# Optimization experiments

Measured on AMD Instinct MI355X. Metric: run time of the kernel, lower is better.

Reference implementation:

```python
import jax, jax.numpy as jnp
import numpy as np

DEPTH = 6; HEADS = 6; DIM = 384; HD = DIM // HEADS
WS = 14; WINDOW_BLOCKS = (0, 1, 3, 4)
IMG = 512; PATCH = 16; GRID = IMG // PATCH        # 32x32 token grid
PRE_GRID = 14                                      # 224 // 16 pretrain grid
SCALE = HD ** -0.5


def layer_norm(x, w, b, eps=1e-5):
    u = x.mean(-1, keepdims=True)
    s = ((x - u) ** 2).mean(-1, keepdims=True)
    return (x - u) / jnp.sqrt(s + eps) * w + b


def get_rel_pos(size, rel_pos):
    # q_size == k_size here; relative coords in [0, 2*size-2]
    coords = jnp.arange(size)[:, None] - jnp.arange(size)[None, :] + (size - 1)
    return rel_pos[coords]  # (size, size, HD)


def attention(x, qkv_w, qkv_b, proj_w, proj_b, rel_h, rel_w):
    B, H, W, C = x.shape
    N = H * W
    qkv = (x.reshape(B, N, C) @ qkv_w.T + qkv_b).reshape(B, N, 3, HEADS, HD)
    qkv = jnp.moveaxis(qkv, 2, 0).transpose(0, 1, 3, 2, 4)  # (3,B,h,N,d)
    q, k, v = qkv[0], qkv[1], qkv[2]
    attn = jnp.einsum('bhqd,bhkd->bhqk', q * SCALE, k)
    # decomposed relative position bias (ViTDet add_decomposed_rel_pos)
    Rh = get_rel_pos(H, rel_h)  # (H,H,d)
    Rw = get_rel_pos(W, rel_w)  # (W,W,d)
    rq = q.reshape(B, HEADS, H, W, HD)
    bias_h = jnp.einsum('bnhwc,hkc->bnhwk', rq, Rh)  # (B,h,H,W,H)
    bias_w = jnp.einsum('bnhwc,wkc->bnhwk', rq, Rw)  # (B,h,H,W,W)
    attn = (attn.reshape(B, HEADS, H, W, H, W)
            + bias_h[..., :, None] + bias_w[..., None, :]).reshape(B, HEADS, N, N)
    attn = jax.nn.softmax(attn, axis=-1)
    out = jnp.einsum('bhqk,bhkd->bhqd', attn, v)
    out = out.transpose(0, 2, 1, 3).reshape(B, H, W, C)
    return out @ proj_w.T + proj_b


def window_partition(x, ws):
    B, H, W, C = x.shape
    pad_h = (ws - H % ws) % ws
    pad_w = (ws - W % ws) % ws
    x = jnp.pad(x, ((0, 0), (0, pad_h), (0, pad_w), (0, 0)))
    Hp, Wp = H + pad_h, W + pad_w
    x = x.reshape(B, Hp // ws, ws, Wp // ws, ws, C)
    x = x.transpose(0, 1, 3, 2, 4, 5).reshape(-1, ws, ws, C)
    return x, Hp, Wp


def window_unpartition(win, ws, Hp, Wp, H, W):
    B = win.shape[0] // ((Hp // ws) * (Wp // ws))
    x = win.reshape(B, Hp // ws, Wp // ws, ws, ws, -1)
    x = x.transpose(0, 1, 3, 2, 4, 5).reshape(B, Hp, Wp, -1)
    return x[:, :H, :W]


def block(x, p, windowed):
    shortcut = x
    x = layer_norm(x, p['n1w'], p['n1b'])
    if windowed:
        H, W = x.shape[1], x.shape[2]
        x, Hp, Wp = window_partition(x, WS)
    x = attention(x, p['qw'], p['qb'], p['pw'], p['pb'], p['rh'], p['rw'])
    if windowed:
        x = window_unpartition(x, WS, Hp, Wp, H, W)
    x = shortcut + x
    h = layer_norm(x, p['n2w'], p['n2b'])
    h = jax.nn.gelu(h @ p['f1w'].T + p['f1b'], approximate=False)
    return x + h @ p['f2w'].T + p['f2b']


def vit_forward(x, patch_w, patch_b, pos_embed, norm1_w, norm1_b, qkv_w, qkv_b,
                proj_w, proj_b, norm2_w, norm2_b, fc1_w, fc1_b, fc2_w, fc2_b,
                rel_pos_h, rel_pos_w):
    y = jax.lax.conv_general_dilated(
        x, patch_w, (PATCH, PATCH), 'VALID',
        dimension_numbers=('NCHW', 'OIHW', 'NCHW'))
    y = y.transpose(0, 2, 3, 1) + patch_b  # (B, GRID, GRID, DIM)
    # abs pos embed: bicubic resize from pretrain 14x14 grid to 32x32
    pos = pos_embed.reshape(1, PRE_GRID, PRE_GRID, DIM)
    pos = jax.image.resize(pos, (1, GRID, GRID, DIM), 'bicubic')
    y = y + pos
    for i in range(DEPTH):
        windowed = i in WINDOW_BLOCKS
        L = 2 * WS - 1 if windowed else 2 * GRID - 1
        p = dict(n1w=norm1_w[i], n1b=norm1_b[i], qw=qkv_w[i], qb=qkv_b[i],
                 pw=proj_w[i], pb=proj_b[i], rh=rel_pos_h[i, :L], rw=rel_pos_w[i, :L],
                 n2w=norm2_w[i], n2b=norm2_b[i], f1w=fc1_w[i], f1b=fc1_b[i],
                 f2w=fc2_w[i], f2b=fc2_b[i])
        y = block(y, p, windowed)
    return y.transpose(0, 3, 1, 2)  # (B, DIM, GRID, GRID) 'last_feat'


def setup_inputs() -> dict:
    key = jax.random.key(0)
    ks = jax.random.split(key, 10)
    B = 4
    std = 0.02
    f32 = jnp.float32
    return {
        'x': jax.random.normal(ks[0], (B, 3, IMG, IMG), f32),
        'patch_w': jax.random.normal(ks[1], (DIM, 3, PATCH, PATCH), f32) * 0.05,
        'patch_b': jnp.zeros((DIM,), f32),
        'pos_embed': jax.random.normal(ks[2], (1, PRE_GRID * PRE_GRID, DIM), f32) * std,
        'norm1_w': jnp.ones((DEPTH, DIM), f32),
        'norm1_b': jnp.zeros((DEPTH, DIM), f32),
        'qkv_w': jax.random.normal(ks[3], (DEPTH, 3 * DIM, DIM), f32) * std,
        'qkv_b': jnp.zeros((DEPTH, 3 * DIM), f32),
        'proj_w': jax.random.normal(ks[4], (DEPTH, DIM, DIM), f32) * std,
        'proj_b': jnp.zeros((DEPTH, DIM), f32),
        'norm2_w': jnp.ones((DEPTH, DIM), f32),
        'norm2_b': jnp.zeros((DEPTH, DIM), f32),
        'fc1_w': jax.random.normal(ks[5], (DEPTH, 4 * DIM, DIM), f32) * std,
        'fc1_b': jnp.zeros((DEPTH, 4 * DIM), f32),
        'fc2_w': jax.random.normal(ks[6], (DEPTH, DIM, 4 * DIM), f32) * std,
        'fc2_b': jnp.zeros((DEPTH, DIM), f32),
        'rel_pos_h': jax.random.normal(ks[7], (DEPTH, 2 * GRID - 1, HD), f32) * std,
        'rel_pos_w': jax.random.normal(ks[8], (DEPTH, 2 * GRID - 1, HD), f32) * std,
    }


def reference(x, patch_w, patch_b, pos_embed, norm1_w, norm1_b, qkv_w, qkv_b,
              proj_w, proj_b, norm2_w, norm2_b, fc1_w, fc1_b, fc2_w, fc2_b,
              rel_pos_h, rel_pos_w):
    return vit_forward(x, patch_w, patch_b, pos_embed, norm1_w, norm1_b, qkv_w, qkv_b,
                       proj_w, proj_b, norm2_w, norm2_b, fc1_w, fc1_b, fc2_w, fc2_b,
                       rel_pos_h, rel_pos_w)
```

## Files before the change

### kernel.cpp

```cpp
#include <hip/hip_runtime.h>
#include <hip/hip_bf16.h>
#include <math.h>

#define B_SZ 4
#define DIM 384
#define HEADS 6
#define HD 64
#define NTOK 4096
#define WS 14
#define NWIN 36
#define WTOK 196

typedef unsigned short u16;
typedef __bf16 bf16_t;
typedef bf16_t bf16x8 __attribute__((ext_vector_type(8)));
typedef float f32x4 __attribute__((ext_vector_type(4)));

__device__ __forceinline__ float bf2f(unsigned u) { return __uint_as_float(u << 16); }
__device__ __forceinline__ u16 f2bf(float f) {
    unsigned u = __float_as_uint(f);
    unsigned r = (u + 0x7fffu + ((u >> 16) & 1u)) >> 16;
    return (u16)r;
}
__device__ __forceinline__ unsigned pk2bf(float a, float b) {
    __hip_bfloat162 h = __float22bfloat162_rn(make_float2(a, b));
    unsigned r; __builtin_memcpy(&r, &h, 4); return r;
}

__device__ __forceinline__ void ldsload16(const u16* g, u16* l) {
    __builtin_amdgcn_global_load_lds(
        (const __attribute__((address_space(1))) unsigned int*)g,
        (__attribute__((address_space(3))) unsigned int*)l, 16, 0, 0);
}

__device__ __forceinline__ int swz(int r) { return (r ^ (r >> 2)) & 3; }

__device__ inline float cubic_keys(float x) {
    x = fabsf(x);
    if (x <= 1.f) return ((1.5f * x - 2.5f) * x) * x + 1.f;
    if (x < 2.f)  return ((-0.5f * x + 2.5f) * x - 4.f) * x + 2.f;
    return 0.f;
}

__global__ __launch_bounds__(256) void setup_kernel(
        const float* __restrict__ p0, const float* __restrict__ p1,
        const float* __restrict__ p2, const float* __restrict__ p3,
        const float* __restrict__ p4, const float* __restrict__ p5,
        u16* __restrict__ wb, const float* __restrict__ pe,
        float* __restrict__ posr, const float* __restrict__ x,
        u16* __restrict__ col) {
    int i = (blockIdx.x * 256 + threadIdx.x) * 4;
    if (i < 10918656) {
        const float* s; int off;
        if      (i <   294912) { s = p0; off = 0; }
        else if (i <  2949120) { s = p1; off = 294912; }
        else if (i <  3833856) { s = p2; off = 2949120; }
        else if (i <  7372800) { s = p3; off = 3833856; }
        else if (i < 10911744) { s = p4; off = 7372800; }
        else                   { s = p5; off = 10911744; }
        float4 v = *(const float4*)(s + (i - off));
        u16 o[4] = { f2bf(v.x), f2bf(v.y), f2bf(v.z), f2bf(v.w) };
        *(uint2*)(wb + i) = *(const uint2*)o;
        return;
    }
    i -= 10918656;
    if (i < 393216) {
        int c = i % 384;
        int g = i / 384;
        int gy = g / 32, gx = g % 32;
        float wy[14], wx[14];
        float sy = (gy + 0.5f) * (14.f / 32.f) - 0.5f;
        float sx = (gx + 0.5f) * (14.f / 32.f) - 0.5f;
        float toty = 0.f, totx = 0.f;
        #pragma unroll
        for (int k = 0; k < 14; ++k) {
            wy[k] = cubic_keys(sy - (float)k); toty += wy[k];
            wx[k] = cubic_keys(sx - (float)k); totx += wx[k];
        }
        float4 acc = {0.f, 0.f, 0.f, 0.f};
        #pragma unroll 1
        for (int iy = 0; iy < 14; ++iy) {
            if (wy[iy] == 0.f) continue;
            float4 row = {0.f, 0.f, 0.f, 0.f};
            for (int ix = 0; ix < 14; ++ix) {
                if (wx[ix] == 0.f) continue;
                float4 pv = *(const float4*)(pe + (iy * 14 + ix) * 384 + c);
                row.x += wx[ix] * pv.x; row.y += wx[ix] * pv.y;
                row.z += wx[ix] * pv.z; row.w += wx[ix] * pv.w;
            }
            acc.x += wy[iy] * row.x; acc.y += wy[iy] * row.y;
            acc.z += wy[iy] * row.z; acc.w += wy[iy] * row.w;
        }
        float inv = 1.f / (toty * totx);
        acc.x *= inv; acc.y *= inv; acc.z *= inv; acc.w *= inv;
        *(float4*)(posr + i) = acc;
        return;
    }
    i -= 393216;
    if (i < 3145728) {
        int kk = i % 768;
        int p  = i / 768;
        int b  = p / 1024;
        int ph = (p % 1024) / 32;
        int pw = p % 32;
        int c = kk / 256;
        int r = kk % 256;
        int ii = r / 16, j = r % 16;
        float4 v = *(const float4*)(x + (size_t)b * 3 * 512 * 512 +
                                    (size_t)c * 512 * 512 +
                                    (size_t)(ph * 16 + ii) * 512 + (pw * 16 + j));
        u16 o[4] = { f2bf(v.x), f2bf(v.y), f2bf(v.z), f2bf(v.w) };
        *(uint2*)(col + i) = *(const uint2*)o;
    }
}

__global__ __launch_bounds__(256) void epi_ln_kernel(const float* __restrict__ P,
        const float* __restrict__ bias, const float* __restrict__ posr,
        float* __restrict__ y, int addy, int nsk,
        const float* __restrict__ lw, const float* __restrict__ lb,
        u16* __restrict__ lnout)
{
    int tok = blockIdx.x * 4 + (threadIdx.x >> 6);
    int t = threadIdx.x & 63;
    size_t base = (size_t)tok * 384;
    float v[6];
    float s = 0.f;
    #pragma unroll
    for (int i = 0; i < 6; ++i) {
        int c = t + 64 * i;
        float val = bias[c];
        #pragma unroll 1
        for (int sk = 0; sk < nsk; ++sk)
            val += P[(size_t)sk * 1572864 + base + c];
        if (posr) val += posr[(size_t)(tok & 1023) * 384 + c];
        if (addy) val += y[base + c];
        v[i] = val; s += val;
    }
    #pragma unroll
    for (int i = 0; i < 6; ++i) y[base + t + 64 * i] = v[i];
    if (!lnout) return;
    #pragma unroll
    for (int off = 32; off > 0; off >>= 1) s += __shfl_xor(s, off);
    float mean = s * (1.f / 384.f);
    float vs = 0.f;
    #pragma unroll
    for (int i = 0; i < 6; ++i) { float d = v[i] - mean; vs += d * d; }
    #pragma unroll
    for (int off = 32; off > 0; off >>= 1) vs += __shfl_xor(vs, off);
    float inv = rsqrtf(vs * (1.f / 384.f) + 1e-5f);
    u16* orow = lnout + base;
    #pragma unroll
    for (int i = 0; i < 6; ++i) {
        int c = t + 64 * i;
        orow[c] = f2bf((v[i] - mean) * inv * lw[c] + lb[c]);
    }
}

__global__ __launch_bounds__(256) void out_transpose(const float* __restrict__ y,
        float* __restrict__ outT)
{
    __shared__ float T[64][65];
    int c0 = blockIdx.x * 64, m0 = blockIdx.y * 64;
    int t = threadIdx.x;
    int cl = t & 63, wv = t >> 6;
    #pragma unroll
    for (int r = 0; r < 16; ++r) {
        int ml = wv * 16 + r;
        T[ml][cl] = y[(size_t)(m0 + ml) * 384 + c0 + cl];
    }
    __syncthreads();
    int b = m0 >> 10, g0 = m0 & 1023;
    int gl = t & 63;
    #pragma unroll
    for (int r = 0; r < 16; ++r) {
        int ccl = wv * 16 + r;
        outT[((size_t)(b * 384 + c0 + ccl)) * 1024 + g0 + gl] = T[gl][ccl];
    }
}

__global__ __launch_bounds__(256) void mfma_gemm4(
        const u16* __restrict__ A, const u16* __restrict__ Wt,
        const float* __restrict__ bias,
        float* __restrict__ outf, u16* __restrict__ outb,
        float* __restrict__ outp,
        int M, int N, int K, int act, int ksplit)
{
    __shared__ u16 As[2][8192];
    __shared__ u16 Bs[2][4096];
    int t = threadIdx.x;
    int lane = t & 63, wave = t >> 6;
    int wm = (wave >> 1) * 64, wn = (wave & 1) * 32;
    int m0 = blockIdx.y * 128, n0 = blockIdx.x * 64;
    int ks = blockIdx.z * ksplit;

    int r0 = t >> 2,        c0 = ((t & 3) ^ swz(t >> 2)) * 8;
    int r1 = 64 + (t >> 2), c1 = ((t & 3) ^ swz(64 + (t >> 2))) * 8;
    const u16* a0 = A + (size_t)(m0 + r0) * K + c0;
    const u16* a1 = A + (size_t)(m0 + r1) * K + c1;
    const u16* b0 = Wt + (size_t)(n0 + r0) * K + c0;

    auto stage = [&](int k0, int buf) {
        ldsload16(a0 + k0,      &As[buf][wave * 512]);
        ldsload16(a1 + k0,      &As[buf][2048 + wave * 512]);
        ldsload16(b0 + k0,      &Bs[buf][wave * 512]);
        ldsload16(a0 + k0 + 32, &As[buf][4096 + wave * 512]);
        ldsload16(a1 + k0 + 32, &As[buf][6144 + wave * 512]);
        ldsload16(b0 + k0 + 32, &Bs[buf][2048 + wave * 512]);
    };

    f32x4 acc[4][2] = {};
    int row_a = wm + (lane & 15);
    int row_b = wn + (lane & 15);
    int lq = lane >> 4;
    int nchunks = ksplit / 64;

    stage(ks, 0);
    __syncthreads();

    for (int ci = 0; ci < nchunks; ++ci) {
        int p = ci & 1;
        bool pref = (ci + 1 < nchunks);
        if (pref) stage(ks + (ci + 1) * 64, 1 - p);
        #pragma unroll
        for (int hf = 0; hf < 2; ++hf) {
            bf16x8 af[4], bfr[2];
            #pragma unroll
            for (int i = 0; i < 4; ++i) {
                int r = row_a + i * 16;
                af[i] = *(const bf16x8*)&As[p][hf * 4096 + r * 32 + ((lq ^ swz(r)) * 8)];
            }
            #pragma unroll
            for (int j = 0; j < 2; ++j) {
                int r = row_b + j * 16;
                bfr[j] = *(const bf16x8*)&Bs[p][hf * 2048 + r * 32 + ((lq ^ swz(r)) * 8)];
            }
            #pragma unroll
            for (int i = 0; i < 4; ++i)
                #pragma unroll
                for (int j = 0; j < 2; ++j)
                    acc[i][j] = __builtin_amdgcn_mfma_f32_16x16x32_bf16(
                        af[i], bfr[j], acc[i][j], 0, 0, 0);
        }
        if (pref) __syncthreads();
    }

    int colq = lane & 15, rowq = (lane >> 4) * 4;
    if (outp) {
        float* pp = outp + (size_t)blockIdx.z * M * N;
        #pragma unroll
        for (int i = 0; i < 4; ++i) {
            #pragma unroll
            for (int rr = 0; rr < 4; ++rr) {
                int m = m0 + wm + i * 16 + rowq + rr;
                size_t mo = (size_t)m * N;
                #pragma unroll
                for (int j = 0; j < 2; ++j) {
                    int n = n0 + wn + j * 16 + colq;
                    pp[mo + n] = acc[i][j][rr];
                }
            }
        }
        return;
    }
    #pragma unroll
    for (int i = 0; i < 4; ++i) {
        #pragma unroll
        for (int rr = 0; rr < 4; ++rr) {
            int m = m0 + wm + i * 16 + rowq + rr;
            size_t mo = (size_t)m * N;
            #pragma unroll
            for (int j = 0; j < 2; ++j) {
                int n = n0 + wn + j * 16 + colq;
                float v = acc[i][j][rr] + bias[n];
                if (act)  v = 0.5f * v * (1.f + erff(v * 0.70710678118654752f));
                if (outf) outf[mo + n] = v;
                if (outb) outb[mo + n] = f2bf(v);
            }
        }
    }
}

template<int N, int W>
__global__ __launch_bounds__(256) void attn_mfma(const u16* __restrict__ qkv,
        const u16* __restrict__ qkb, const float* __restrict__ rh,
        const float* __restrict__ rw, u16* __restrict__ outb,
        float* __restrict__ opart, float* __restrict__ lpart)
{
    constexpr int JS = (W == 32) ? 64 : 32;
    constexpr int L  = (W == 32) ? 63 : 27;
    constexpr int CTR = W - 1;
    constexpr int KSPAN = (W == 32) ? 512 : 224;
    constexpr int NKT = KSPAN / 32;
    __shared__ u16 KV[11776];
    __shared__ u16 bhl[64 * 66];
    __shared__ u16 bwl[64 * 66];
    __shared__ u16 Qt[64 * 66];

    u16* Pb = KV + 9216;
    u16* Rt = KV;

    int t = threadIdx.x, lane = t & 63, wave = t >> 6;
    int quad = lane >> 4, l15 = lane & 15;
    int uh = blockIdx.x, qb0 = blockIdx.y * 64;
    int z = (W == 32) ? blockIdx.z : 0;
    int kstart = z * KSPAN;
    int h = uh % HEADS, u = uh / HEADS;
    size_t tbase = (size_t)u * 1024;
    int wb_ = u / 9, wr = u - wb_ * 9;
    int wy = wr / 3, wx = wr - wy * 3;

    auto tok14 = [&](int iy, int ix) -> const u16* {
        int gy = wy * WS + iy, gx = wx * WS + ix;
        if (gy < 32 && gx < 32)
            return qkv + (size_t)(wb_ * 1024 + gy * 32 + gx) * 1152;
        return qkb;
    };
    auto rowptr = [&](int lq2) -> const u16* {
        if constexpr (W == 32) {
            return qkv + (tbase + lq2) * 1152;
        } else {
            int iy = lq2 / WS, ix = lq2 - iy * WS;
            return tok14(iy, ix);
        }
    };

    {
        int q = t & 63, ch0 = (t >> 6) * 16;
        int qc = qb0 + q; if (qc >= N) qc = N - 1;
        const u16* qp = rowptr(qc) + h * 64 + ch0;
        uint4 a = *(const uint4*)qp;
        uint4 b = *(const uint4*)(qp + 8);
        u16 vals[16];
        *(uint4*)vals = a; *(uint4*)(vals + 8) = b;
        #pragma unroll
        for (int c = 0; c < 16; ++c)
            Qt[(ch0 + c) * 66 + q] = ((qb0 + q) < N) ? vals[c] : (u16)0;
    }

    #pragma unroll
    for (int table = 0; table < 2; ++table) {
        __syncthreads();
        const float* tab = table ? rw : rh;
        for (int idx = t; idx < JS * 8; idx += 256) {
            int j = idx >> 3, cc0 = (idx & 7) * 8;
            u16 tmp[8];
            if (j < L) {
                const float* src = tab + (size_t)j * 64 + cc0;
                #pragma unroll
                for (int c = 0; c < 8; ++c) tmp[c] = f2bf(src[c]);
            } else {
                #pragma unroll
                for (int c = 0; c < 8; ++c) tmp[c] = 0;
            }
            *(uint4*)&Rt[j * 72 + cc0] = *(uint4*)tmp;
        }
        __syncthreads();
        if (wave < JS / 16) {
            int jt = wave;
            bf16x8 af0 = *(const bf16x8*)&Rt[(jt * 16 + l15) * 72 + quad * 8];
            bf16x8 af1 = *(const bf16x8*)&Rt[(jt * 16 + l15) * 72 + 32 + quad * 8];
            u16* dst = table ? bwl : bhl;
            #pragma unroll
            for (int qt = 0; qt < 4; ++qt) {
                bf16x8 qf0, qf1;
                u16* p0 = (u16*)&qf0; u16* p1 = (u16*)&qf1;
                #pragma unroll
                for (int zz = 0; zz < 8; ++zz) {
                    p0[zz] = Qt[(quad * 8 + zz) * 66 + qt * 16 + l15];
                    p1[zz] = Qt[(32 + quad * 8 + zz) * 66 + qt * 16 + l15];
                }
                f32x4 acc = {};
                acc = __builtin_amdgcn_mfma_f32_16x16x32_bf16(af0, qf0, acc, 0, 0, 0);
                acc = __builtin_amdgcn_mfma_f32_16x16x32_bf16(af1, qf1, acc, 0, 0, 0);
                #pragma unroll
                for (int r = 0; r < 4; ++r)
                    dst[(qt * 16 + l15) * 66 + jt * 16 + quad * 4 + r] = f2bf(acc[r]);
            }
        }
    }
    __syncthreads();

    int skey = (wave * 64 + lane) >> 3;
    int sc8  = ((wave * 64 + lane) & 7) ^ (skey & 7);
    int vkey = t & 31, vch0 = (t >> 5) * 8;
    int siy = 0, six = 0, viy = 0, vix = 0;
    if constexpr (W != 32) {
        int k0 = kstart + skey;
        siy = k0 / WS; six = k0 - siy * WS;
        int k1 = kstart + vkey;
        viy = k1 / WS; vix = k1 - viy * WS;
    }
    auto adv = [](int& iy, int& ix) { ix += 4; iy += 2; if (ix >= WS) { ix -= WS; ++iy; } };

    {
        const u16* kp = (W == 32) ? qkv + (tbase + kstart + skey) * 1152
                                  : tok14(siy, six);
        ldsload16(kp + 384 + h * 64 + sc8 * 8, KV + wave * 512);
        const u16* vp = (W == 32) ? qkv + (tbase + kstart + vkey) * 1152
                                  : tok14(viy, vix);
        uint4 vv = *(const uint4*)(vp + 768 + h * 64 + vch0);
        u16 tmp[8]; *(uint4*)tmp = vv;
        u16* vdst = KV + 4096;
        #pragma unroll
        for (int c = 0; c < 8; ++c) vdst[(vch0 + c) * 40 + vkey] = tmp[c];
        if constexpr (W != 32) { adv(siy, six); adv(viy, vix); }
    }

    bf16x8 qf[2];
    #pragma unroll
    for (int hc = 0; hc < 2; ++hc) {
        u16* qv = (u16*)&qf[hc];
        #pragma unroll
        for (int j = 0; j < 8; ++j)
            qv[j] = Qt[(hc * 32 + quad * 8 + j) * 66 + wave * 16 + l15];
    }
    int qme = wave * 16 + l15;
    bool wactive = (W == 32) ? true : ((qb0 + wave * 16) < N);
    int qq = qb0 + qme; if (qq >= N) qq = N - 1;
    int qh = qq / W, qw = qq - qh * W;
    float bwreg[2][4];
    int kh_[2][4], kw_[2][4];
    #pragma unroll
    for (int kc2 = 0; kc2 < 2; ++kc2)
        #pragma unroll
        for (int r = 0; r < 4; ++r) {
            int keyl = kc2 * 16 + quad * 4 + r;
            if constexpr (W == 32) {
                bwreg[kc2][r] = bf2f(bwl[qme * 66 + (qw - keyl + CTR)]);
            } else {
                kh_[kc2][r] = keyl / WS;
                kw_[kc2][r] = keyl - kh_[kc2][r] * WS;
            }
        }

    f32x4 of[4] = {};
    float lsum = 0.f;
    __syncthreads();

    for (int kt = 0; kt < NKT; ++kt) {
        int kb = kstart + kt * 32;
        int p = kt & 1;
        const u16* ksp = KV + p * 2048;
        const u16* vtp = KV + 4096 + p * 2560;
        bool pref = (kt + 1 < NKT);
        uint4 vpref;
        if (pref) {
            const u16* kp = (W == 32) ? qkv + (tbase + kb + 32 + skey) * 1152
                                      : tok14(siy, six);
            ldsload16(kp + 384 + h * 64 + sc8 * 8, KV + (1 - p) * 2048 + wave * 512);
            const u16* vp = (W == 32) ? qkv + (tbase + kb + 32 + vkey) * 1152
                                      : tok14(viy, vix);
            vpref = *(const uint4*)(vp + 768 + h * 64 + vch0);
            if constexpr (W != 32) { adv(siy, six); adv(viy, vix); }
        }

        if (wactive) {
            f32x4 st[2] = {};
            #pragma unroll
            for (int hc = 0; hc < 2; ++hc) {
                #pragma unroll
                for (int kc2 = 0; kc2 < 2; ++kc2) {
                    int key = kc2 * 16 + l15;
                    int c8 = hc * 4 + quad;
                    int pp = key * 8 + (c8 ^ (key & 7));
                    bf16x8 kf = *(const bf16x8*)&ksp[pp * 8];
                    st[kc2] = __builtin_amdgcn_mfma_f32_16x16x32_bf16(
                        kf, qf[hc], st[kc2], 0, 0, 0);
                }
            }
            float bh_t = 0.f;
            if constexpr (W == 32) bh_t = bf2f(bhl[qme * 66 + (qh - (kb >> 5) + CTR)]);
            #pragma unroll
            for (int kc2 = 0; kc2 < 2; ++kc2) {
                float pv4[4];
                #pragma unroll
                for (int r = 0; r < 4; ++r) {
                    int keyl = kc2 * 16 + quad * 4 + r;
                    float b;
                    if constexpr (W == 32) {
                        b = bh_t + bwreg[kc2][r];
                    } else {
                        b = bf2f(bhl[qme * 66 + (qh - kh_[kc2][r] + CTR)]) +
                            bf2f(bwl[qme * 66 + (qw - kw_[kc2][r] + CTR)]);
                    }
                    float pv = __expf(fmaf(st[kc2][r], 0.125f, b));
                    if (kb + keyl >= N) pv = 0.f;
                    lsum += pv;
                    pv4[r] = pv;
                }
                uint2 pk;
                pk.x = pk2bf(pv4[0], pv4[1]);
                pk.y = pk2bf(pv4[2], pv4[3]);
                *(uint2*)&Pb[wave * 640 + l15 * 40 + kc2 * 16 + quad * 4] = pk;
            }
            if constexpr (W != 32) {
                #pragma unroll
                for (int kc2 = 0; kc2 < 2; ++kc2)
                    #pragma unroll
                    for (int r = 0; r < 4; ++r) {
                        kw_[kc2][r] += 4; kh_[kc2][r] += 2;
                        if (kw_[kc2][r] >= WS) { kw_[kc2][r] -= WS; ++kh_[kc2][r]; }
                    }
            }
            bf16x8 pf = *(const bf16x8*)&Pb[wave * 640 + l15 * 40 + quad * 8];
            #pragma unroll
            for (int ca = 0; ca < 4; ++ca) {
                bf16x8 vf = *(const bf16x8*)&vtp[(ca * 16 + l15) * 40 + quad * 8];
                of[ca] = __builtin_amdgcn_mfma_f32_16x16x32_bf16(
                    vf, pf, of[ca], 0, 0, 0);
            }
        }

        if (pref) {
            u16 tmp[8]; *(uint4*)tmp = vpref;
            u16* vdst = KV + 4096 + (1 - p) * 2560;
            #pragma unroll
            for (int c = 0; c < 8; ++c) vdst[(vch0 + c) * 40 + vkey] = tmp[c];
            __syncthreads();
        }
    }

    lsum += __shfl_xor(lsum, 16);
    lsum += __shfl_xor(lsum, 32);
    int q = qb0 + qme;
    if constexpr (W == 32) {
        size_t ridx = (size_t)z * 24576 + (size_t)uh * 1024 + q;
        float* op = opart + ridx * 64;
        #pragma unroll
        for (int ca = 0; ca < 4; ++ca)
            *(float4*)&op[ca * 16 + quad * 4] = (float4){of[ca][0], of[ca][1],
                                                         of[ca][2], of[ca][3]};
        if (quad == 0) lpart[ridx] = lsum;
    } else {
        float inv = 1.f / lsum;
        if (q < N) {
            int iy = q / WS, ix = q - iy * WS;
            int gy = wy * WS + iy, gx = wx * WS + ix;
            if (gy >= 32 || gx >= 32) return;
            u16* op = outb + (size_t)(wb_ * 1024 + gy * 32 + gx) * 384 + h * 64;
            #pragma unroll
            for (int ca = 0; ca < 4; ++ca) {
                uint2 pk;
                pk.x = pk2bf(of[ca][0] * inv, of[ca][1] * inv);
                pk.y = pk2bf(of[ca][2] * inv, of[ca][3] * inv);
                *(uint2*)&op[ca * 16 + quad * 4] = pk;
            }
        }
    }
}

__global__ __launch_bounds__(256) void attn_merge_kernel(const float* __restrict__ O,
        const float* __restrict__ Lp, u16* __restrict__ attb)
{
    int t = threadIdx.x;
    int idx = blockIdx.x * 4 + (t >> 6);
    int ch = t & 63;
    float o = O[(size_t)idx * 64 + ch] + O[((size_t)24576 + idx) * 64 + ch];
    float l = Lp[idx] + Lp[24576 + idx];
    int uh = idx >> 10, q = idx & 1023;
    int u = uh / 6, h = uh - u * 6;
    attb[((size_t)(u * 1024 + q)) * 384 + h * 64 + ch] = f2bf(o / l);
}

static inline void launch_gemm(const u16* A, const u16* W, const float* bias,
                               float* outf, u16* outb,
                               int M, int N, int K, int act, hipStream_t s) {
    dim3 g(N / 64, M / 128, 1);
    mfma_gemm4<<<g, 256, 0, s>>>(A, W, bias, outf, outb, nullptr, M, N, K, act, K);
}

static inline void launch_gemm_sk(const u16* A, const u16* W, float* P,
                                  int M, int N, int K, int SK, hipStream_t s) {
    dim3 g(N / 64, M / 128, SK);
    mfma_gemm4<<<g, 256, 0, s>>>(A, W, nullptr, nullptr, nullptr, P,
                                 M, N, K, 0, K / SK);
}

extern "C" void kernel_launch(void* const* d_in, const int* in_sizes, int n_in,
                              void* d_out, int out_size, void* d_ws, size_t ws_size,
                              hipStream_t stream) {
    const float* x      = (const float*)d_in[0];
    const float* patchw = (const float*)d_in[1];
    const float* patchb = (const float*)d_in[2];
    const float* pos    = (const float*)d_in[3];
    const float* n1w    = (const float*)d_in[4];
    const float* n1b    = (const float*)d_in[5];
    const float* qkvw   = (const float*)d_in[6];
    const float* qkvb   = (const float*)d_in[7];
    const float* pw     = (const float*)d_in[8];
    const float* pb     = (const float*)d_in[9];
    const float* n2w    = (const float*)d_in[10];
    const float* n2b    = (const float*)d_in[11];
    const float* f1w    = (const float*)d_in[12];
    const float* f1b    = (const float*)d_in[13];
    const float* f2w    = (const float*)d_in[14];
    const float* f2b    = (const float*)d_in[15];
    const float* rph    = (const float*)d_in[16];
    const float* rpw    = (const float*)d_in[17];
    float* out = (float*)d_out;

    float* y   = (float*)d_ws;
    u16* attb  = (u16*)(y + 1572864);
    u16* mlpb  = attb + 1572864;
    u16* lnb   = mlpb + 6291456;
    u16* qkvx  = lnb + 1572864;
    u16* rsrv  = qkvx + 4718592;
    u16* wb    = rsrv + 7864320;
    float* posr = (float*)(wb + 10918656);

    u16* colb  = rsrv;
    float* P_patch = (float*)attb;
    float* P_pf    = (float*)qkvx;
    float* Opart   = (float*)mlpb;
    float* Lpart   = (float*)lnb;

    u16* wb_patch = wb;
    u16* wb_qkv   = wb + 294912;
    u16* wb_pw    = wb + 2949120;
    u16* wb_f1    = wb + 3833856;
    u16* wb_f2    = wb + 7372800;
    u16* wqb      = wb + 10911744;

    setup_kernel<<<(14457600 / 4 + 255) / 256, 256, 0, stream>>>(
        patchw, qkvw, pw, f1w, f2w, qkvb, wb, pos, posr, x, colb);

    launch_gemm_sk(colb, wb_patch, P_patch, NTOK, 384, 768, 2, stream);
    epi_ln_kernel<<<1024, 256, 0, stream>>>(P_patch, patchb, posr, y, 0, 2,
                                            n1w, n1b, lnb);

    for (int i = 0; i < 6; ++i) {
        bool windowed = (i == 0 || i == 1 || i == 3 || i == 4);
        const float* rh = rph + (size_t)i * 63 * 64;
        const float* rw = rpw + (size_t)i * 63 * 64;
        launch_gemm(lnb, wb_qkv + (size_t)i * 442368, qkvb + i * 1152,
                    nullptr, qkvx, NTOK, 1152, 384, 0, stream);
        if (windowed) {
            attn_mfma<WTOK, WS><<<dim3(NWIN * HEADS, 4, 1), 256, 0, stream>>>(
                qkvx, wqb + i * 1152, rh, rw, attb, nullptr, nullptr);
        } else {
            attn_mfma<1024, 32><<<dim3(B_SZ * HEADS, 16, 2), 256, 0, stream>>>(
                qkvx, wqb + i * 1152, rh, rw, nullptr, Opart, Lpart);
            attn_merge_kernel<<<6144, 256, 0, stream>>>(Opart, Lpart, attb);
        }
        launch_gemm_sk(attb, wb_pw + (size_t)i * 147456, P_pf,
                       NTOK, 384, 384, 2, stream);
        epi_ln_kernel<<<1024, 256, 0, stream>>>(P_pf, pb + i * 384, nullptr, y, 1, 2,
                                                n2w + i * 384, n2b + i * 384, lnb);
        launch_gemm(lnb, wb_f1 + (size_t)i * 589824, f1b + i * 1536,
                    nullptr, mlpb, NTOK, 1536, 384, 1, stream);
        launch_gemm_sk(mlpb, wb_f2 + (size_t)i * 589824, P_pf,
                       NTOK, 384, 1536, 2, stream);
        if (i < 5)
            epi_ln_kernel<<<1024, 256, 0, stream>>>(P_pf, f2b + i * 384, nullptr, y,
                                                    1, 2, n1w + (i + 1) * 384,
                                                    n1b + (i + 1) * 384, lnb);
        else {
            epi_ln_kernel<<<1024, 256, 0, stream>>>(P_pf, f2b + i * 384, nullptr, y,
                                                    1, 2, nullptr, nullptr, nullptr);
            out_transpose<<<dim3(6, 64), 256, 0, stream>>>(y, out);
        }
    }
}
```

Before: 747.9 us.

## Replace split-K GEMMs with 64x64-tile GEMM that fuses bias and residual epilogue

```diff
diff --git a/kernel.cpp b/kernel.cpp
--- a/kernel.cpp
+++ b/kernel.cpp
@@ -114,9 +114,7 @@
     }
 }
 
-__global__ __launch_bounds__(256) void epi_ln_kernel(const float* __restrict__ P,
-        const float* __restrict__ bias, const float* __restrict__ posr,
-        float* __restrict__ y, int addy, int nsk,
+__global__ __launch_bounds__(256) void ln_kernel(const float* __restrict__ y,
         const float* __restrict__ lw, const float* __restrict__ lb,
         u16* __restrict__ lnout)
 {
@@ -127,18 +125,8 @@
     float s = 0.f;
     #pragma unroll
     for (int i = 0; i < 6; ++i) {
-        int c = t + 64 * i;
-        float val = bias[c];
-        #pragma unroll 1
-        for (int sk = 0; sk < nsk; ++sk)
-            val += P[(size_t)sk * 1572864 + base + c];
-        if (posr) val += posr[(size_t)(tok & 1023) * 384 + c];
-        if (addy) val += y[base + c];
-        v[i] = val; s += val;
-    }
-    #pragma unroll
-    for (int i = 0; i < 6; ++i) y[base + t + 64 * i] = v[i];
-    if (!lnout) return;
+        v[i] = y[base + t + 64 * i]; s += v[i];
+    }
     #pragma unroll
     for (int off = 32; off > 0; off >>= 1) s += __shfl_xor(s, off);
     float mean = s * (1.f / 384.f);
@@ -181,9 +169,8 @@
 __global__ __launch_bounds__(256) void mfma_gemm4(
         const u16* __restrict__ A, const u16* __restrict__ Wt,
         const float* __restrict__ bias,
-        float* __restrict__ outf, u16* __restrict__ outb,
-        float* __restrict__ outp,
-        int M, int N, int K, int act, int ksplit)
+        u16* __restrict__ outb,
+        int M, int N, int K, int act)
 {
     __shared__ u16 As[2][8192];
     __shared__ u16 Bs[2][4096];
@@ -191,7 +178,6 @@
     int lane = t & 63, wave = t >> 6;
     int wm = (wave >> 1) * 64, wn = (wave & 1) * 32;
     int m0 = blockIdx.y * 128, n0 = blockIdx.x * 64;
-    int ks = blockIdx.z * ksplit;
 
     int r0 = t >> 2,        c0 = ((t & 3) ^ swz(t >> 2)) * 8;
     int r1 = 64 + (t >> 2), c1 = ((t & 3) ^ swz(64 + (t >> 2))) * 8;
@@ -212,15 +198,15 @@
     int row_a = wm + (lane & 15);
     int row_b = wn + (lane & 15);
     int lq = lane >> 4;
-    int nchunks = ksplit / 64;
-
-    stage(ks, 0);
+    int nchunks = K / 64;
+
+    stage(0, 0);
     __syncthreads();
 
     for (int ci = 0; ci < nchunks; ++ci) {
         int p = ci & 1;
         bool pref = (ci + 1 < nchunks);
-        if (pref) stage(ks + (ci + 1) * 64, 1 - p);
+        if (pref) stage((ci + 1) * 64, 1 - p);
         #pragma unroll
         for (int hf = 0; hf < 2; ++hf) {
             bf16x8 af[4], bfr[2];
@@ -245,23 +231,6 @@
     }
 
     int colq = lane & 15, rowq = (lane >> 4) * 4;
-    if (outp) {
-        float* pp = outp + (size_t)blockIdx.z * M * N;
-        #pragma unroll
-        for (int i = 0; i < 4; ++i) {
-            #pragma unroll
-            for (int rr = 0; rr < 4; ++rr) {
-                int m = m0 + wm + i * 16 + rowq + rr;
-                size_t mo = (size_t)m * N;
-                #pragma unroll
-                for (int j = 0; j < 2; ++j) {
-                    int n = n0 + wn + j * 16 + colq;
-                    pp[mo + n] = acc[i][j][rr];
-                }
-            }
-        }
-        return;
-    }
     #pragma unroll
     for (int i = 0; i < 4; ++i) {
         #pragma unroll
@@ -273,8 +242,85 @@
                 int n = n0 + wn + j * 16 + colq;
                 float v = acc[i][j][rr] + bias[n];
                 if (act)  v = 0.5f * v * (1.f + erff(v * 0.70710678118654752f));
-                if (outf) outf[mo + n] = v;
-                if (outb) outb[mo + n] = f2bf(v);
+                outb[mo + n] = f2bf(v);
+            }
+        }
+    }
+}
+
+__global__ __launch_bounds__(256) void mfma_gemm64(
+        const u16* __restrict__ A, const u16* __restrict__ Wt,
+        const float* __restrict__ bias, const float* __restrict__ posr,
+        float* __restrict__ y, int addy, int M, int N, int K)
+{
+    __shared__ u16 As[2][4096];
+    __shared__ u16 Bs[2][4096];
+    int t = threadIdx.x;
+    int lane = t & 63, wave = t >> 6;
+    int wm = (wave >> 1) * 32, wn = (wave & 1) * 32;
+    int m0 = blockIdx.y * 64, n0 = blockIdx.x * 64;
+
+    int r0 = t >> 2, c0 = ((t & 3) ^ swz(t >> 2)) * 8;
+    const u16* a0 = A + (size_t)(m0 + r0) * K + c0;
+    const u16* b0 = Wt + (size_t)(n0 + r0) * K + c0;
+
+    auto stage = [&](int k0, int buf) {
+        ldsload16(a0 + k0,      &As[buf][wave * 512]);
+        ldsload16(b0 + k0,      &Bs[buf][wave * 512]);
+        ldsload16(a0 + k0 + 32, &As[buf][2048 + wave * 512]);
+        ldsload16(b0 + k0 + 32, &Bs[buf][2048 + wave * 512]);
+    };
+
+    f32x4 acc[2][2] = {};
+    int row_a = wm + (lane & 15);
+    int row_b = wn + (lane & 15);
+    int lq = lane >> 4;
+    int nchunks = K / 64;
+
+    stage(0, 0);
+    __syncthreads();
+
+    for (int ci = 0; ci < nchunks; ++ci) {
+        int p = ci & 1;
+        bool pref = (ci + 1 < nchunks);
+        if (pref) stage((ci + 1) * 64, 1 - p);
+        #pragma unroll
+        for (int hf = 0; hf < 2; ++hf) {
+            bf16x8 af[2], bfr[2];
+            #pragma unroll
+            for (int i = 0; i < 2; ++i) {
+                int r = row_a + i * 16;
+                af[i] = *(const bf16x8*)&As[p][hf * 2048 + r * 32 + ((lq ^ swz(r)) * 8)];
+            }
+            #pragma unroll
+            for (int j = 0; j < 2; ++j) {
+                int r = row_b + j * 16;
+                bfr[j] = *(const bf16x8*)&Bs[p][hf * 2048 + r * 32 + ((lq ^ swz(r)) * 8)];
+            }
+            #pragma unroll
+            for (int i = 0; i < 2; ++i)
+                #pragma unroll
+                for (int j = 0; j < 2; ++j)
+                    acc[i][j] = __builtin_amdgcn_mfma_f32_16x16x32_bf16(
+                        af[i], bfr[j], acc[i][j], 0, 0, 0);
+        }
+        if (pref) __syncthreads();
+    }
+
+    int colq = lane & 15, rowq = (lane >> 4) * 4;
+    #pragma unroll
+    for (int i = 0; i < 2; ++i) {
+        #pragma unroll
+        for (int rr = 0; rr < 4; ++rr) {
+            int m = m0 + wm + i * 16 + rowq + rr;
+            size_t mo = (size_t)m * N;
+            #pragma unroll
+            for (int j = 0; j < 2; ++j) {
+                int n = n0 + wn + j * 16 + colq;
+                float v = acc[i][j][rr] + bias[n];
+                if (posr) v += posr[(size_t)(m & 1023) * 384 + n];
+                if (addy) v += y[mo + n];
+                y[mo + n] = v;
             }
         }
     }
@@ -563,17 +609,17 @@
 }
 
 static inline void launch_gemm(const u16* A, const u16* W, const float* bias,
-                               float* outf, u16* outb,
-                               int M, int N, int K, int act, hipStream_t s) {
+                               u16* outb, int M, int N, int K, int act,
+                               hipStream_t s) {
     dim3 g(N / 64, M / 128, 1);
-    mfma_gemm4<<<g, 256, 0, s>>>(A, W, bias, outf, outb, nullptr, M, N, K, act, K);
-}
-
-static inline void launch_gemm_sk(const u16* A, const u16* W, float* P,
-                                  int M, int N, int K, int SK, hipStream_t s) {
-    dim3 g(N / 64, M / 128, SK);
-    mfma_gemm4<<<g, 256, 0, s>>>(A, W, nullptr, nullptr, nullptr, P,
-                                 M, N, K, 0, K / SK);
+    mfma_gemm4<<<g, 256, 0, s>>>(A, W, bias, outb, M, N, K, act);
+}
+
+static inline void launch_gemm64(const u16* A, const u16* W, const float* bias,
+                                 const float* posr, float* y, int addy,
+                                 int M, int N, int K, hipStream_t s) {
+    dim3 g(N / 64, M / 64, 1);
+    mfma_gemm64<<<g, 256, 0, s>>>(A, W, bias, posr, y, addy, M, N, K);
 }
 
 extern "C" void kernel_launch(void* const* d_in, const int* in_sizes, int n_in,
@@ -609,8 +655,6 @@
     float* posr = (float*)(wb + 10918656);
 
     u16* colb  = rsrv;
-    float* P_patch = (float*)attb;
-    float* P_pf    = (float*)qkvx;
     float* Opart   = (float*)mlpb;
     float* Lpart   = (float*)lnb;
 
@@ -624,16 +668,15 @@
     setup_kernel<<<(14457600 / 4 + 255) / 256, 256, 0, stream>>>(
         patchw, qkvw, pw, f1w, f2w, qkvb, wb, pos, posr, x, colb);
 
-    launch_gemm_sk(colb, wb_patch, P_patch, NTOK, 384, 768, 2, stream);
-    epi_ln_kernel<<<1024, 256, 0, stream>>>(P_patch, patchb, posr, y, 0, 2,
-                                            n1w, n1b, lnb);
+    launch_gemm64(colb, wb_patch, patchb, posr, y, 0, NTOK, 384, 768, stream);
+    ln_kernel<<<1024, 256, 0, stream>>>(y, n1w, n1b, lnb);
 
     for (int i = 0; i < 6; ++i) {
         bool windowed = (i == 0 || i == 1 || i == 3 || i == 4);
         const float* rh = rph + (size_t)i * 63 * 64;
         const float* rw = rpw + (size_t)i * 63 * 64;
         launch_gemm(lnb, wb_qkv + (size_t)i * 442368, qkvb + i * 1152,
-                    nullptr, qkvx, NTOK, 1152, 384, 0, stream);
+                    qkvx, NTOK, 1152, 384, 0, stream);
         if (windowed) {
             attn_mfma<WTOK, WS><<<dim3(NWIN * HEADS, 4, 1), 256, 0, stream>>>(
                 qkvx, wqb + i * 1152, rh, rw, attb, nullptr, nullptr);
@@ -642,22 +685,17 @@
                 qkvx, wqb + i * 1152, rh, rw, nullptr, Opart, Lpart);
             attn_merge_kernel<<<6144, 256, 0, stream>>>(Opart, Lpart, attb);
         }
-        launch_gemm_sk(attb, wb_pw + (size_t)i * 147456, P_pf,
-                       NTOK, 384, 384, 2, stream);
-        epi_ln_kernel<<<1024, 256, 0, stream>>>(P_pf, pb + i * 384, nullptr, y, 1, 2,
-                                                n2w + i * 384, n2b + i * 384, lnb);
+        launch_gemm64(attb, wb_pw + (size_t)i * 147456, pb + i * 384,
+                      nullptr, y, 1, NTOK, 384, 384, stream);
+        ln_kernel<<<1024, 256, 0, stream>>>(y, n2w + i * 384, n2b + i * 384, lnb);
         launch_gemm(lnb, wb_f1 + (size_t)i * 589824, f1b + i * 1536,
-                    nullptr, mlpb, NTOK, 1536, 384, 1, stream);
-        launch_gemm_sk(mlpb, wb_f2 + (size_t)i * 589824, P_pf,
-                       NTOK, 384, 1536, 2, stream);
+                    mlpb, NTOK, 1536, 384, 1, stream);
+        launch_gemm64(mlpb, wb_f2 + (size_t)i * 589824, f2b + i * 384,
+                      nullptr, y, 1, NTOK, 384, 1536, stream);
         if (i < 5)
-            epi_ln_kernel<<<1024, 256, 0, stream>>>(P_pf, f2b + i * 384, nullptr, y,
-                                                    1, 2, n1w + (i + 1) * 384,
-                                                    n1b + (i + 1) * 384, lnb);
-        else {
-            epi_ln_kernel<<<1024, 256, 0, stream>>>(P_pf, f2b + i * 384, nullptr, y,
-                                                    1, 2, nullptr, nullptr, nullptr);
+            ln_kernel<<<1024, 256, 0, stream>>>(y, n1w + (i + 1) * 384,
+                                                n1b + (i + 1) * 384, lnb);
+        else
             out_transpose<<<dim3(6, 64), 256, 0, stream>>>(y, out);
-        }
-    }
-}
+    }
+}
```

After: 710.6 us. -5.0%, faster.
